# Kernel optimization log

Measured on AMD Instinct MI355X. Metric: run time of the kernel, lower is better.

Reference implementation:

```python
import jax, jax.numpy as jnp
import numpy as np

TOP_K = 2  # config['num_experts_per_tok']


def setup_inputs() -> dict:
    key = jax.random.key(0)
    ks = jax.random.split(key, 8)
    B, S, H, E, I, IS = 2, 2048, 1024, 8, 2048, 4096
    w = 0.02
    return {
        "hidden_states": jax.random.normal(ks[0], (B, S, H), dtype=jnp.float32),
        "router_w": jax.random.normal(ks[1], (E, H), dtype=jnp.float32) * w,  # nn.Linear(H, E) weight
        "Wg": jax.random.normal(ks[2], (E, H, I), dtype=jnp.float32) * w,  # gate_proj per expert
        "Wu": jax.random.normal(ks[3], (E, H, I), dtype=jnp.float32) * w,  # up_proj per expert
        "Wd": jax.random.normal(ks[4], (E, I, H), dtype=jnp.float32) * w,  # down_proj per expert
        "Sg": jax.random.normal(ks[5], (H, IS), dtype=jnp.float32) * w,   # shared expert gate
        "Su": jax.random.normal(ks[6], (H, IS), dtype=jnp.float32) * w,   # shared expert up
        "Sd": jax.random.normal(ks[7], (IS, H), dtype=jnp.float32) * w,   # shared expert down
    }


def reference(hidden_states, router_w, Wg, Wu, Wd, Sg, Su, Sd):
    B, S, H = hidden_states.shape
    E = router_w.shape[0]
    x = hidden_states.reshape(-1, H)                       # [T, H]

    # Router: top-k over logits, softmax over selected logits (as in torch code)
    logits = x @ router_w.T                                # [T, E]
    topv, sel = jax.lax.top_k(logits, TOP_K)               # [T, K]
    rw = jax.nn.softmax(topv, axis=-1)                     # [T, K]
    # Per-token combine weight for each expert (0 if not selected)
    cw = jnp.sum(jax.nn.one_hot(sel, E, dtype=x.dtype) * rw[..., None], axis=1)  # [T, E]

    # Expert SwiGLU (dense over experts, weighted combine == gather/GEMM/scatter math)
    gate = jax.nn.silu(jnp.einsum('th,ehi->tei', x, Wg))   # [T, E, I]
    up = jnp.einsum('th,ehi->tei', x, Wu)                  # [T, E, I]
    expout = jnp.einsum('tei,eih->teh', gate * up, Wd)     # [T, E, H]
    moe = jnp.einsum('te,teh->th', cw, expout)             # [T, H]

    # Shared expert (always active)
    shared = (jax.nn.silu(x @ Sg) * (x @ Su)) @ Sd         # [T, H]

    out = (moe + shared).reshape(B, S, H)
    router_z_loss = jnp.asarray(0.0, dtype=x.dtype)        # eval mode: z-loss is 0.0
    return out, router_z_loss
```

## Files before the change

### kernel.cpp

```cpp
#include <hip/hip_runtime.h>
#include <hip/hip_bf16.h>
#include <stdint.h>


typedef __attribute__((ext_vector_type(8))) short bf16x8;
typedef __attribute__((ext_vector_type(4))) float f32x4;
typedef unsigned short u16;

static constexpr int Tt  = 4096;
static constexpr int Hd  = 1024;
static constexpr int NE  = 8;
static constexpr int Id  = 2048;
static constexpr int ISd = 4096;
static constexpr int NR  = Tt * 2;
static constexpr int BM = 128, BN = 128, BN1 = 64, BK = 64;
static constexpr int MAXT = NR / BM + NE;
static constexpr int G1_SH = (Tt / BM) * (ISd / BN1);
static constexpr int G1_EX = MAXT * (Id / BN1);
static constexpr int G2_SH = 8 * (Tt / BM) * 2;
static constexpr int G2_EX = 8 * MAXT;

__device__ __forceinline__ u16 f2bf(float f) {
  union { float f; uint32_t u; } v; v.f = f;
  uint32_t u = v.u;
  u += 0x7fffu + ((u >> 16) & 1u);
  return (u16)(u >> 16);
}

__device__ __forceinline__ void ld16(void* l, const void* g) {
  __builtin_amdgcn_global_load_lds((const __attribute__((address_space(1))) void*)g,
                                   (__attribute__((address_space(3))) void*)l, 16, 0, 0);
}


__global__ void k_cvt(const float* __restrict__ s, u16* __restrict__ d, int n) {
  int i = (blockIdx.x * 256 + threadIdx.x) * 8;
  if (i >= n) return;
  float4 a = *(const float4*)(s + i);
  float4 b = *(const float4*)(s + i + 4);
  union { u16 h[8]; uint4 v; } o;
  o.h[0] = f2bf(a.x); o.h[1] = f2bf(a.y); o.h[2] = f2bf(a.z); o.h[3] = f2bf(a.w);
  o.h[4] = f2bf(b.x); o.h[5] = f2bf(b.y); o.h[6] = f2bf(b.z); o.h[7] = f2bf(b.w);
  *(uint4*)(d + i) = o.v;
}

__global__ __launch_bounds__(256)
void k_tcvt(const float* __restrict__ s0, u16* __restrict__ d0,
            const float* __restrict__ s1, u16* __restrict__ d1,
            const float* __restrict__ s2, u16* __restrict__ d2,
            const float* __restrict__ s3, u16* __restrict__ d3,
            const float* __restrict__ s4, u16* __restrict__ d4,
            const float* __restrict__ s5, u16* __restrict__ d5) {
  constexpr int ST[6] = {0, 4096, 8192, 12288, 13312, 14336};
  constexpr int KS[6] = {1024, 1024, 2048, 1024, 1024, 4096};
  constexpr int NS[6] = {2048, 2048, 1024, 4096, 4096, 1024};
  int bid = blockIdx.x;
  int seg = 0;
  #pragma unroll
  for (int i = 1; i < 6; i++) if (bid >= ST[i]) seg = i;
  const float* S; u16* D;
  switch (seg) {
    case 0: S = s0; D = d0; break;
    case 1: S = s1; D = d1; break;
    case 2: S = s2; D = d2; break;
    case 3: S = s3; D = d3; break;
    case 4: S = s4; D = d4; break;
    default: S = s5; D = d5; break;
  }
  int K = KS[seg], N = NS[seg];
  int lb = bid - ST[seg];
  int perz = (N >> 6) * (K >> 6);
  int z = lb / perz, r = lb - z * perz;
  int bx = r % (N >> 6), by = r / (N >> 6);
  S += (size_t)z * K * N; D += (size_t)z * K * N;
  int n0 = bx * 64, k0 = by * 64;

  __shared__ float sm[64][65];
  int tid = threadIdx.x;
  int rr = tid >> 4, cc = (tid & 15) * 4;
  #pragma unroll
  for (int i = 0; i < 4; i++) {
    float4 v = *(const float4*)&S[(size_t)(k0 + i * 16 + rr) * N + n0 + cc];
    sm[i * 16 + rr][cc] = v.x; sm[i * 16 + rr][cc + 1] = v.y;
    sm[i * 16 + rr][cc + 2] = v.z; sm[i * 16 + rr][cc + 3] = v.w;
  }
  __syncthreads();
  int nn = tid >> 3, kc = (tid & 7) * 8;
  #pragma unroll
  for (int i = 0; i < 2; i++) {
    int n = i * 32 + nn;
    union { u16 h[8]; uint4 v; } o;
    #pragma unroll
    for (int t = 0; t < 8; t++) o.h[t] = f2bf(sm[kc + t][n]);
    *(uint4*)&D[(size_t)(n0 + n) * K + k0 + kc] = o.v;
  }
}


__global__ __launch_bounds__(256)
void k_router(const float* __restrict__ x, const float* __restrict__ rwm,
              int* __restrict__ sel, float* __restrict__ wts,
              int* __restrict__ counts) {
  __shared__ float w[NE * Hd];
  __shared__ int lcnt[NE];
  int tid = threadIdx.x;
  if (tid < NE) lcnt[tid] = 0;
  #pragma unroll
  for (int i = 0; i < 8; i++) {
    int idx = (i * 256 + tid) * 4;
    *(float4*)&w[idx] = *(const float4*)&rwm[idx];
  }
  __syncthreads();
  int tok = blockIdx.x * 16 + (tid >> 4);
  int part = tid & 15;
  const float* xt = x + (size_t)tok * Hd;
  float p[NE] = {};
  #pragma unroll
  for (int j = 0; j < 16; j++) {
    int off = j * 64 + part * 4;
    float4 v = *(const float4*)&xt[off];
    #pragma unroll
    for (int e = 0; e < NE; e++) {
      float4 wv = *(const float4*)&w[e * Hd + off];
      p[e] += v.x * wv.x + v.y * wv.y + v.z * wv.z + v.w * wv.w;
    }
  }
  #pragma unroll
  for (int e = 0; e < NE; e++)
    #pragma unroll
    for (int o = 1; o < 16; o <<= 1)
      p[e] += __shfl_xor(p[e], o, 64);
  if (part == 0) {
    int e0 = 0;
    for (int e = 1; e < NE; e++) if (p[e] > p[e0]) e0 = e;
    int e1 = -1;
    for (int e = 0; e < NE; e++) { if (e == e0) continue; if (e1 < 0 || p[e] > p[e1]) e1 = e; }
    float w0 = 1.f / (1.f + expf(p[e1] - p[e0]));
    sel[tok * 2] = e0; sel[tok * 2 + 1] = e1;
    wts[tok * 2] = w0; wts[tok * 2 + 1] = 1.f - w0;
    atomicAdd(&lcnt[e0], 1); atomicAdd(&lcnt[e1], 1);
  }
  __syncthreads();
  if (tid < NE) atomicAdd(&counts[tid], lcnt[tid]);
}

__global__ void k_assign(const int* __restrict__ sel, const float* __restrict__ wts,
                         const int* __restrict__ counts, int* __restrict__ cur,
                         int* __restrict__ rowtok, float* __restrict__ roww) {
  int t = blockIdx.x * 256 + threadIdx.x;
  if (t >= Tt) return;
  int offs[NE];
  int a = 0;
  #pragma unroll
  for (int e = 0; e < NE; e++) { offs[e] = a; a += counts[e]; }
  #pragma unroll
  for (int k = 0; k < 2; k++) {
    int e = sel[t * 2 + k];
    int r = offs[e] + atomicAdd(&cur[e], 1);
    rowtok[r] = t; roww[r] = wts[t * 2 + k];
  }
}


__device__ __forceinline__ bool tile_map(const int* counts, int slot,
                                         int& rowbase, int& mval, int& e_out) {
  int acc = 0, base = 0, e = -1;
  for (int i = 0; i < NE; i++) {
    int c = counts[i];
    int nt = (c + BM - 1) / BM;
    if (e < 0 && slot < acc + nt) {
      int tl = slot - acc;
      e = i;
      rowbase = base + tl * BM;
      int rem = c - tl * BM;
      mval = rem < BM ? rem : BM;
    }
    acc += nt; base += c;
  }
  e_out = e;
  return e >= 0;
}


__global__ __launch_bounds__(256, 3)
void k_gemm1(const u16* __restrict__ A,
             const u16* __restrict__ Sgt, const u16* __restrict__ Sut, u16* __restrict__ hs,
             const u16* __restrict__ Wgt, const u16* __restrict__ Wut, u16* __restrict__ h,
             const int* __restrict__ counts, const int* __restrict__ rowtok) {
  constexpr int KD = Hd;
  int bid = blockIdx.x;
  bool gather;
  const u16 *B1g, *B2g; u16* Ho;
  int NOUT, n, mt, rowbase, mval, eb = 0;
  if (bid < G1_SH) {
    gather = false; NOUT = ISd; B1g = Sgt; B2g = Sut; Ho = hs;
    int xcd = bid & 7, idx = bid >> 3;
    n = xcd * 8 + (idx & 7); mt = idx >> 3;
    rowbase = mt * BM; mval = BM;
  } else {
    gather = true; NOUT = Id; Ho = h;
    int b2 = bid - G1_SH;
    int xcd = b2 & 7, idx = b2 >> 3;
    n = xcd * 4 + (idx & 3); mt = idx >> 2;
    if (!tile_map(counts, mt, rowbase, mval, eb)) return;
    size_t bmat = (size_t)eb * Id * KD;
    B1g = Wgt + bmat; B2g = Wut + bmat;
  }
  __shared__ u16 As[BM * BK], Bs1[BN1 * BK], Bs2[BN1 * BK];
  const int tid = threadIdx.x, w = tid >> 6, l = tid & 63;
  const int lr = l >> 3, cg = (l & 7) ^ lr;

  const u16* gp[8];
  u16* lp[8];
  if (w < 2) {
    #pragma unroll
    for (int j = 0; j < 8; j++) {
      int r = w * 64 + j * 8 + lr;
      int rr = (r < mval) ? r : 0;
      int arow = gather ? rowtok[rowbase + rr] : (rowbase + rr);
      gp[j] = A + (size_t)arow * KD + cg * 8;
      lp[j] = As + (w * 64 + j * 8) * BK;
    }
  } else if (w == 2) {
    #pragma unroll
    for (int j = 0; j < 8; j++) {
      int r = j * 8 + lr;
      gp[j] = B1g + (size_t)(n * BN1 + r) * KD + cg * 8;
      lp[j] = Bs1 + (j * 8) * BK;
    }
  } else {
    #pragma unroll
    for (int j = 0; j < 8; j++) {
      int r = j * 8 + lr;
      gp[j] = B2g + (size_t)(n * BN1 + r) * KD + cg * 8;
      lp[j] = Bs2 + (j * 8) * BK;
    }
  }
  const int wm = w >> 1, wn = w & 1, q = l >> 4, rl = l & 15;
  const int r7 = rl & 7;
  f32x4 aG[4][2] = {}, aU[4][2] = {};

  for (int k0 = 0; k0 < KD; k0 += BK) {
    __syncthreads();
    #pragma unroll
    for (int j = 0; j < 8; j++) ld16(lp[j], gp[j] + k0);
    __syncthreads();
    #pragma unroll
    for (int kk = 0; kk < 2; kk++) {
      bf16x8 af[4], bf1[2], bf2[2];
      #pragma unroll
      for (int i = 0; i < 4; i++)
        af[i] = *(const bf16x8*)(As + (wm * 64 + i * 16 + rl) * BK + ((kk * 4 + q) ^ r7) * 8);
      #pragma unroll
      for (int i = 0; i < 2; i++) {
        bf1[i] = *(const bf16x8*)(Bs1 + (wn * 32 + i * 16 + rl) * BK + ((kk * 4 + q) ^ r7) * 8);
        bf2[i] = *(const bf16x8*)(Bs2 + (wn * 32 + i * 16 + rl) * BK + ((kk * 4 + q) ^ r7) * 8);
      }
      #pragma unroll
      for (int a = 0; a < 4; a++)
        #pragma unroll
        for (int b = 0; b < 2; b++) {
          aG[a][b] = __builtin_amdgcn_mfma_f32_16x16x32_bf16(af[a], bf1[b], aG[a][b], 0, 0, 0);
          aU[a][b] = __builtin_amdgcn_mfma_f32_16x16x32_bf16(af[a], bf2[b], aU[a][b], 0, 0, 0);
        }
    }
  }
  #pragma unroll
  for (int a = 0; a < 4; a++) {
    #pragma unroll
    for (int r = 0; r < 4; r++) {
      int row = wm * 64 + a * 16 + q * 4 + r;
      if (row < mval) {
        size_t ro = (size_t)(rowbase + row) * NOUT;
        #pragma unroll
        for (int b = 0; b < 2; b++) {
          int c = n * BN1 + wn * 32 + b * 16 + rl;
          float g = aG[a][b][r], u = aU[a][b][r];
          Ho[ro + c] = f2bf(g / (1.f + __expf(-g)) * u);
        }
      }
    }
  }
}

__global__ __launch_bounds__(256, 3)
void k_gemm2(const u16* __restrict__ hs, const u16* __restrict__ Sdt,
             const u16* __restrict__ h, const u16* __restrict__ Wdt,
             float* __restrict__ out,
             const int* __restrict__ counts, const int* __restrict__ rowtok,
             const float* __restrict__ roww) {
  int bid = blockIdx.x;
  bool gather;
  const u16 *A, *Bg;
  int n, rowbase, mval, eb = 0, kstart, KDrow;
  if (bid < G2_SH) {
    gather = false; KDrow = ISd;
    n = bid & 7;
    int idx = bid >> 3;
    int mt = idx & 31, kz = idx >> 5;
    rowbase = mt * BM; mval = BM;
    kstart = kz * (ISd / 2);
    A = hs; Bg = Sdt;
  } else {
    gather = true; KDrow = Id;
    int b2 = bid - G2_SH;
    n = b2 & 7;
    int mt = b2 >> 3;
    if (!tile_map(counts, mt, rowbase, mval, eb)) return;
    kstart = 0;
    A = h; Bg = Wdt + (size_t)eb * Hd * Id;
  }
  __shared__ u16 As[BM * BK], Bs[BN * BK];
  const int tid = threadIdx.x, w = tid >> 6, l = tid & 63;
  const int lr = l >> 3, cg = (l & 7) ^ lr;

  const u16* gp[8];
  u16* lp[8];
  if (w < 2) {
    #pragma unroll
    for (int j = 0; j < 8; j++) {
      int r = w * 64 + j * 8 + lr;
      int rr = (r < mval) ? r : 0;
      gp[j] = A + (size_t)(rowbase + rr) * KDrow + cg * 8;
      lp[j] = As + (w * 64 + j * 8) * BK;
    }
  } else {
    #pragma unroll
    for (int j = 0; j < 8; j++) {
      int r = (w - 2) * 64 + j * 8 + lr;
      gp[j] = Bg + (size_t)(n * BN + r) * KDrow + cg * 8;
      lp[j] = Bs + ((w - 2) * 64 + j * 8) * BK;
    }
  }
  const int wm = w >> 1, wn = w & 1, q = l >> 4, rl = l & 15;
  const int r7 = rl & 7;
  f32x4 acc[4][4] = {};

  const int kend = kstart + 2048;
  for (int k0 = kstart; k0 < kend; k0 += BK) {
    __syncthreads();
    #pragma unroll
    for (int j = 0; j < 8; j++) ld16(lp[j], gp[j] + k0);
    __syncthreads();
    #pragma unroll
    for (int kk = 0; kk < 2; kk++) {
      bf16x8 af[4], bf[4];
      #pragma unroll
      for (int i = 0; i < 4; i++) {
        af[i] = *(const bf16x8*)(As + (wm * 64 + i * 16 + rl) * BK + ((kk * 4 + q) ^ r7) * 8);
        bf[i] = *(const bf16x8*)(Bs + (wn * 64 + i * 16 + rl) * BK + ((kk * 4 + q) ^ r7) * 8);
      }
      #pragma unroll
      for (int a = 0; a < 4; a++)
        #pragma unroll
        for (int b = 0; b < 4; b++)
          acc[a][b] = __builtin_amdgcn_mfma_f32_16x16x32_bf16(af[a], bf[b], acc[a][b], 0, 0, 0);
    }
  }
  #pragma unroll
  for (int a = 0; a < 4; a++) {
    #pragma unroll
    for (int r = 0; r < 4; r++) {
      int row = wm * 64 + a * 16 + q * 4 + r;
      if (row < mval) {
        int grow = rowbase + row;
        float wt = 1.f;
        size_t o;
        if (gather) { o = (size_t)rowtok[grow] * Hd; wt = roww[grow]; }
        else o = (size_t)grow * Hd;
        #pragma unroll
        for (int b = 0; b < 4; b++) {
          int c = n * BN + wn * 64 + b * 16 + rl;
          atomicAdd(&out[o + c], wt * acc[a][b][r]);
        }
      }
    }
  }
}


extern "C" void kernel_launch(void* const* d_in, const int* in_sizes, int n_in,
                              void* d_out, int out_size, void* d_ws, size_t ws_size,
                              hipStream_t stream) {
  const float* x   = (const float*)d_in[0];
  const float* rwm = (const float*)d_in[1];
  const float* Wg  = (const float*)d_in[2];
  const float* Wu  = (const float*)d_in[3];
  const float* Wd  = (const float*)d_in[4];
  const float* Sg  = (const float*)d_in[5];
  const float* Su  = (const float*)d_in[6];
  const float* Sd  = (const float*)d_in[7];
  float* out = (float*)d_out;

  uint8_t* p = (uint8_t*)d_ws;
  auto take = [&](size_t bytes) { uint8_t* r = p; p += ((bytes + 255) & ~(size_t)255); return r; };
  u16* xb   = (u16*)take((size_t)Tt * Hd * 2);
  u16* Wgt  = (u16*)take((size_t)NE * Id * Hd * 2);
  u16* Wut  = (u16*)take((size_t)NE * Id * Hd * 2);
  u16* Wdt  = (u16*)take((size_t)NE * Hd * Id * 2);
  u16* Sgt  = (u16*)take((size_t)ISd * Hd * 2);
  u16* Sut  = (u16*)take((size_t)ISd * Hd * 2);
  u16* Sdt  = (u16*)take((size_t)Hd * ISd * 2);
  u16* hs   = (u16*)take((size_t)Tt * ISd * 2);
  u16* h    = (u16*)take((size_t)NR * Id * 2);
  int*   sel    = (int*)take(Tt * 2 * 4);
  float* wts    = (float*)take(Tt * 2 * 4);
  int*   rowtok = (int*)take(NR * 4);
  float* roww   = (float*)take(NR * 4);
  int*   ctrl   = (int*)take(2 * NE * 4);
  int* counts = ctrl, *cur = ctrl + NE;

  hipMemsetAsync(ctrl, 0, 2 * NE * 4, stream);
  hipMemsetAsync(out, 0, (size_t)out_size * 4, stream);

  k_cvt<<<(Tt * Hd / 8 + 255) / 256, 256, 0, stream>>>(x, xb, Tt * Hd);
  k_tcvt<<<15360, 256, 0, stream>>>(Wg, Wgt, Wu, Wut, Wd, Wdt, Sg, Sgt, Su, Sut, Sd, Sdt);
  k_router<<<Tt / 16, 256, 0, stream>>>(x, rwm, sel, wts, counts);
  k_assign<<<Tt / 256, 256, 0, stream>>>(sel, wts, counts, cur, rowtok, roww);

  k_gemm1<<<G1_SH + G1_EX, 256, 0, stream>>>(xb, Sgt, Sut, hs, Wgt, Wut, h, counts, rowtok);
  k_gemm2<<<G2_SH + G2_EX, 256, 0, stream>>>(hs, Sdt, h, Wdt, out, counts, rowtok, roww);
}
```

Baseline: 606.0 us.

## Switch GEMMs to 32x32x16 MFMA and fuse x bf16 conversion into router

Both grouped GEMM kernels now use 32x32x16 bf16 MFMA tiles instead of 16x16x32, which cuts LDS fragment reads per MFMA and changes the accumulator layout and epilogue indexing. The separate activation fp32-to-bf16 conversion kernel is removed, and the router, which already reads x, now writes the bf16 copy. The larger MFMA shape raises per-instruction work and reuse but changes register pressure and the epilogue store/atomic pattern.

```diff
diff --git a/kernel.cpp b/kernel.cpp
--- a/kernel.cpp
+++ b/kernel.cpp
@@ -4,7 +4,7 @@
 
 
 typedef __attribute__((ext_vector_type(8))) short bf16x8;
-typedef __attribute__((ext_vector_type(4))) float f32x4;
+typedef __attribute__((ext_vector_type(16))) float f32x16;
 typedef unsigned short u16;
 
 static constexpr int Tt  = 4096;
@@ -33,17 +33,6 @@
 }
 
 
-__global__ void k_cvt(const float* __restrict__ s, u16* __restrict__ d, int n) {
-  int i = (blockIdx.x * 256 + threadIdx.x) * 8;
-  if (i >= n) return;
-  float4 a = *(const float4*)(s + i);
-  float4 b = *(const float4*)(s + i + 4);
-  union { u16 h[8]; uint4 v; } o;
-  o.h[0] = f2bf(a.x); o.h[1] = f2bf(a.y); o.h[2] = f2bf(a.z); o.h[3] = f2bf(a.w);
-  o.h[4] = f2bf(b.x); o.h[5] = f2bf(b.y); o.h[6] = f2bf(b.z); o.h[7] = f2bf(b.w);
-  *(uint4*)(d + i) = o.v;
-}
-
 __global__ __launch_bounds__(256)
 void k_tcvt(const float* __restrict__ s0, u16* __restrict__ d0,
             const float* __restrict__ s1, u16* __restrict__ d1,
@@ -99,6 +88,7 @@
 
 __global__ __launch_bounds__(256)
 void k_router(const float* __restrict__ x, const float* __restrict__ rwm,
+              u16* __restrict__ xb,
               int* __restrict__ sel, float* __restrict__ wts,
               int* __restrict__ counts) {
   __shared__ float w[NE * Hd];
@@ -114,11 +104,15 @@
   int tok = blockIdx.x * 16 + (tid >> 4);
   int part = tid & 15;
   const float* xt = x + (size_t)tok * Hd;
+  u16* xbt = xb + (size_t)tok * Hd;
   float p[NE] = {};
   #pragma unroll
   for (int j = 0; j < 16; j++) {
     int off = j * 64 + part * 4;
     float4 v = *(const float4*)&xt[off];
+    ushort4 o;
+    o.x = f2bf(v.x); o.y = f2bf(v.y); o.z = f2bf(v.z); o.w = f2bf(v.w);
+    *(ushort4*)&xbt[off] = o;
     #pragma unroll
     for (int e = 0; e < NE; e++) {
       float4 wv = *(const float4*)&w[e * Hd + off];
@@ -180,6 +174,7 @@
   e_out = e;
   return e >= 0;
 }
+
 
 
 __global__ __launch_bounds__(256, 3)
@@ -236,9 +231,9 @@
       lp[j] = Bs2 + (j * 8) * BK;
     }
   }
-  const int wm = w >> 1, wn = w & 1, q = l >> 4, rl = l & 15;
-  const int r7 = rl & 7;
-  f32x4 aG[4][2] = {}, aU[4][2] = {};
+  const int wm = w >> 1, wn = w & 1;
+  const int l31 = l & 31, lh = l >> 5;
+  f32x16 aG[2] = {}, aU[2] = {};
 
   for (int k0 = 0; k0 < KD; k0 += BK) {
     __syncthreads();
@@ -246,38 +241,35 @@
     for (int j = 0; j < 8; j++) ld16(lp[j], gp[j] + k0);
     __syncthreads();
     #pragma unroll
-    for (int kk = 0; kk < 2; kk++) {
-      bf16x8 af[4], bf1[2], bf2[2];
+    for (int ks = 0; ks < 4; ks++) {
+      int kc = ks * 2 + lh;
+      bf16x8 af[2], bf1, bf2;
       #pragma unroll
-      for (int i = 0; i < 4; i++)
-        af[i] = *(const bf16x8*)(As + (wm * 64 + i * 16 + rl) * BK + ((kk * 4 + q) ^ r7) * 8);
+      for (int mi = 0; mi < 2; mi++) {
+        int row = wm * 64 + mi * 32 + l31;
+        af[mi] = *(const bf16x8*)(As + row * BK + ((kc ^ (row & 7)) * 8));
+      }
+      {
+        int row = wn * 32 + l31;
+        bf1 = *(const bf16x8*)(Bs1 + row * BK + ((kc ^ (row & 7)) * 8));
+        bf2 = *(const bf16x8*)(Bs2 + row * BK + ((kc ^ (row & 7)) * 8));
+      }
       #pragma unroll
-      for (int i = 0; i < 2; i++) {
-        bf1[i] = *(const bf16x8*)(Bs1 + (wn * 32 + i * 16 + rl) * BK + ((kk * 4 + q) ^ r7) * 8);
-        bf2[i] = *(const bf16x8*)(Bs2 + (wn * 32 + i * 16 + rl) * BK + ((kk * 4 + q) ^ r7) * 8);
-      }
-      #pragma unroll
-      for (int a = 0; a < 4; a++)
-        #pragma unroll
-        for (int b = 0; b < 2; b++) {
-          aG[a][b] = __builtin_amdgcn_mfma_f32_16x16x32_bf16(af[a], bf1[b], aG[a][b], 0, 0, 0);
-          aU[a][b] = __builtin_amdgcn_mfma_f32_16x16x32_bf16(af[a], bf2[b], aU[a][b], 0, 0, 0);
-        }
-    }
-  }
-  #pragma unroll
-  for (int a = 0; a < 4; a++) {
-    #pragma unroll
-    for (int r = 0; r < 4; r++) {
-      int row = wm * 64 + a * 16 + q * 4 + r;
+      for (int mi = 0; mi < 2; mi++) {
+        aG[mi] = __builtin_amdgcn_mfma_f32_32x32x16_bf16(af[mi], bf1, aG[mi], 0, 0, 0);
+        aU[mi] = __builtin_amdgcn_mfma_f32_32x32x16_bf16(af[mi], bf2, aU[mi], 0, 0, 0);
+      }
+    }
+  }
+  #pragma unroll
+  for (int mi = 0; mi < 2; mi++) {
+    #pragma unroll
+    for (int reg = 0; reg < 16; reg++) {
+      int row = wm * 64 + mi * 32 + (reg & 3) + 8 * (reg >> 2) + 4 * lh;
       if (row < mval) {
-        size_t ro = (size_t)(rowbase + row) * NOUT;
-        #pragma unroll
-        for (int b = 0; b < 2; b++) {
-          int c = n * BN1 + wn * 32 + b * 16 + rl;
-          float g = aG[a][b][r], u = aU[a][b][r];
-          Ho[ro + c] = f2bf(g / (1.f + __expf(-g)) * u);
-        }
+        int c = n * BN1 + wn * 32 + l31;
+        float g = aG[mi][reg], u = aU[mi][reg];
+        Ho[(size_t)(rowbase + row) * NOUT + c] = f2bf(g / (1.f + __expf(-g)) * u);
       }
     }
   }
@@ -332,9 +324,9 @@
       lp[j] = Bs + ((w - 2) * 64 + j * 8) * BK;
     }
   }
-  const int wm = w >> 1, wn = w & 1, q = l >> 4, rl = l & 15;
-  const int r7 = rl & 7;
-  f32x4 acc[4][4] = {};
+  const int wm = w >> 1, wn = w & 1;
+  const int l31 = l & 31, lh = l >> 5;
+  f32x16 acc[2][2] = {};
 
   const int kend = kstart + 2048;
   for (int k0 = kstart; k0 < kend; k0 += BK) {
@@ -343,25 +335,31 @@
     for (int j = 0; j < 8; j++) ld16(lp[j], gp[j] + k0);
     __syncthreads();
     #pragma unroll
-    for (int kk = 0; kk < 2; kk++) {
-      bf16x8 af[4], bf[4];
+    for (int ks = 0; ks < 4; ks++) {
+      int kc = ks * 2 + lh;
+      bf16x8 af[2], bf[2];
       #pragma unroll
-      for (int i = 0; i < 4; i++) {
-        af[i] = *(const bf16x8*)(As + (wm * 64 + i * 16 + rl) * BK + ((kk * 4 + q) ^ r7) * 8);
-        bf[i] = *(const bf16x8*)(Bs + (wn * 64 + i * 16 + rl) * BK + ((kk * 4 + q) ^ r7) * 8);
+      for (int mi = 0; mi < 2; mi++) {
+        int row = wm * 64 + mi * 32 + l31;
+        af[mi] = *(const bf16x8*)(As + row * BK + ((kc ^ (row & 7)) * 8));
       }
       #pragma unroll
-      for (int a = 0; a < 4; a++)
+      for (int ni = 0; ni < 2; ni++) {
+        int row = wn * 64 + ni * 32 + l31;
+        bf[ni] = *(const bf16x8*)(Bs + row * BK + ((kc ^ (row & 7)) * 8));
+      }
+      #pragma unroll
+      for (int mi = 0; mi < 2; mi++)
         #pragma unroll
-        for (int b = 0; b < 4; b++)
-          acc[a][b] = __builtin_amdgcn_mfma_f32_16x16x32_bf16(af[a], bf[b], acc[a][b], 0, 0, 0);
-    }
-  }
-  #pragma unroll
-  for (int a = 0; a < 4; a++) {
-    #pragma unroll
-    for (int r = 0; r < 4; r++) {
-      int row = wm * 64 + a * 16 + q * 4 + r;
+        for (int ni = 0; ni < 2; ni++)
+          acc[mi][ni] = __builtin_amdgcn_mfma_f32_32x32x16_bf16(af[mi], bf[ni], acc[mi][ni], 0, 0, 0);
+    }
+  }
+  #pragma unroll
+  for (int mi = 0; mi < 2; mi++) {
+    #pragma unroll
+    for (int reg = 0; reg < 16; reg++) {
+      int row = wm * 64 + mi * 32 + (reg & 3) + 8 * (reg >> 2) + 4 * lh;
       if (row < mval) {
         int grow = rowbase + row;
         float wt = 1.f;
@@ -369,9 +367,9 @@
         if (gather) { o = (size_t)rowtok[grow] * Hd; wt = roww[grow]; }
         else o = (size_t)grow * Hd;
         #pragma unroll
-        for (int b = 0; b < 4; b++) {
-          int c = n * BN + wn * 64 + b * 16 + rl;
-          atomicAdd(&out[o + c], wt * acc[a][b][r]);
+        for (int ni = 0; ni < 2; ni++) {
+          int c = n * BN + wn * 64 + ni * 32 + l31;
+          atomicAdd(&out[o + c], wt * acc[mi][ni][reg]);
         }
       }
     }
@@ -413,9 +411,8 @@
   hipMemsetAsync(ctrl, 0, 2 * NE * 4, stream);
   hipMemsetAsync(out, 0, (size_t)out_size * 4, stream);
 
-  k_cvt<<<(Tt * Hd / 8 + 255) / 256, 256, 0, stream>>>(x, xb, Tt * Hd);
   k_tcvt<<<15360, 256, 0, stream>>>(Wg, Wgt, Wu, Wut, Wd, Wdt, Sg, Sgt, Su, Sut, Sd, Sdt);
-  k_router<<<Tt / 16, 256, 0, stream>>>(x, rwm, sel, wts, counts);
+  k_router<<<Tt / 16, 256, 0, stream>>>(x, rwm, xb, sel, wts, counts);
   k_assign<<<Tt / 256, 256, 0, stream>>>(sel, wts, counts, cur, rowtok, roww);
 
   k_gemm1<<<G1_SH + G1_EX, 256, 0, stream>>>(xb, Sgt, Sut, hs, Wgt, Wut, h, counts, rowtok);
```

Measured after the change: 632.4 us. 1.04x slower.
